# Kernel optimization log

Hardware: AMD Instinct MI355X
Metric: run time of the kernel (lower is better)

## Reference

```python
import math
import jax, jax.numpy as jnp
import numpy as np

B, N, C = 2, 2048, 768
H, DH = 12, 64  # num_heads, head_dim


def setup_inputs() -> dict:
    key = jax.random.key(0)
    ks = jax.random.split(key, 5)
    s = 1.0 / math.sqrt(C)  # keep linear outputs O(1)
    return {
        "x": jax.random.normal(ks[0], (B, N, C), jnp.float32),
        "Wq": jax.random.normal(ks[1], (C, C), jnp.float32) * s,
        "bq": jnp.zeros((C,), jnp.float32),
        "Wk": jax.random.normal(ks[2], (C, C), jnp.float32) * s,
        "bk": jnp.zeros((C,), jnp.float32),
        "Wv": jax.random.normal(ks[3], (C, C), jnp.float32) * s,
        "bv": jnp.zeros((C,), jnp.float32),
        "Wp": jax.random.normal(ks[4], (C, C), jnp.float32) * s,
        "bp": jnp.zeros((C,), jnp.float32),
    }


def reference(x, Wq, bq, Wk, bk, Wv, bv, Wp, bp):
    # Linear projections; torch nn.Linear computes x @ W.T + b, here W stored
    # as (in, out) so it's x @ W + b with equivalent math.
    def split(t):  # [B,N,C] -> [B,H,N,DH]
        return t.reshape(B, N, H, DH).transpose(0, 2, 1, 3)

    q = split(x @ Wq + bq)
    k = split(x @ Wk + bk)
    v = split(x @ Wv + bv)
    scale = 1.0 / math.sqrt(DH)
    attn = jnp.einsum("bhqd,bhkd->bhqk", q, k) * scale  # [B,H,N,N]
    attn = jax.nn.softmax(attn, axis=-1)  # attn_drop=0.0 -> identity
    y = jnp.einsum("bhqk,bhkd->bhqd", attn, v)  # [B,H,N,DH]
    y = y.transpose(0, 2, 1, 3).reshape(B, N, C)
    return y @ Wp + bp  # proj_drop=0.0 -> identity
```

## Files before the change

### kernel.cpp

```cpp
#include <hip/hip_runtime.h>


typedef __bf16 bf16_t;
typedef __bf16 bf16x8 __attribute__((ext_vector_type(8)));
typedef __bf16 bf16x4 __attribute__((ext_vector_type(4)));
typedef short  short4_t __attribute__((ext_vector_type(4)));
typedef float  floatx4 __attribute__((ext_vector_type(4)));

#define MFMA32(a, b, c) __builtin_amdgcn_mfma_f32_16x16x32_bf16(a, b, c, 0, 0, 0)
#define MFMA16(a, b, c) __builtin_amdgcn_mfma_f32_16x16x16bf16_1k(a, b, c, 0, 0, 0)

__global__ __launch_bounds__(256) void cvt_x_kernel(const float* __restrict__ x,
                                                    bf16_t* __restrict__ xb) {
  int i = blockIdx.x * 256 + threadIdx.x;
  floatx4 v = ((const floatx4*)x)[i];
  bf16x4 o;
  o[0] = (bf16_t)v[0]; o[1] = (bf16_t)v[1]; o[2] = (bf16_t)v[2]; o[3] = (bf16_t)v[3];
  ((bf16x4*)xb)[i] = o;
}

__global__ __launch_bounds__(256) void cvt_wt_kernel(
    const float* __restrict__ W0, const float* __restrict__ W1,
    const float* __restrict__ W2, const float* __restrict__ W3,
    bf16_t* __restrict__ T0, bf16_t* __restrict__ T1,
    bf16_t* __restrict__ T2, bf16_t* __restrict__ T3) {
  const int z = blockIdx.z;
  const float* W = (z == 0) ? W0 : (z == 1) ? W1 : (z == 2) ? W2 : W3;
  bf16_t* WT = (z == 0) ? T0 : (z == 1) ? T1 : (z == 2) ? T2 : T3;
  __shared__ bf16_t T[64][65];
  const int c = threadIdx.x & 63, r0 = threadIdx.x >> 6;
  const int i0 = blockIdx.y * 64, o0 = blockIdx.x * 64;
#pragma unroll
  for (int p = 0; p < 16; ++p) {
    int r = p * 4 + r0;
    T[r][c] = (bf16_t)W[(i0 + r) * 768 + o0 + c];
  }
  __syncthreads();
#pragma unroll
  for (int p = 0; p < 16; ++p) {
    int r = p * 4 + r0;
    WT[(o0 + r) * 768 + i0 + c] = T[c][r];
  }
}

#define LDPG 72


__global__ __launch_bounds__(256) void gemm_qkv(
    const bf16_t* __restrict__ Xb, const bf16_t* __restrict__ WqT,
    const bf16_t* __restrict__ WkT, const bf16_t* __restrict__ WvT,
    const float* __restrict__ bq, const float* __restrict__ bk,
    const float* __restrict__ bv, bf16_t* __restrict__ qw,
    bf16_t* __restrict__ kw, bf16_t* __restrict__ vtw) {
  __shared__ bf16_t Al[128 * LDPG];
  __shared__ bf16_t Bl[128 * LDPG];
  const int z = blockIdx.z;
  const bf16_t* Wt = (z == 0) ? WqT : (z == 1) ? WkT : WvT;
  const float* bias = (z == 0) ? bq : (z == 1) ? bk : bv;
  const float oscale = (z == 0) ? 0.18033688011112042f : 1.0f;

  const int tid = threadIdx.x, lane = tid & 63, w = tid >> 6;
  const int wr = w >> 1, wc = w & 1;
  const int l15 = lane & 15, quad = lane >> 4;
  const int m0 = blockIdx.y * 128, n0 = blockIdx.x * 128;

  floatx4 acc[4][4] = {};

  for (int kt = 0; kt < 768; kt += 64) {
#pragma unroll
    for (int p = 0; p < 4; ++p) {
      int c = p * 256 + tid;
      int row = c >> 3, qo = (c & 7) * 8;
      *(bf16x8*)&Al[row * LDPG + qo] = *(const bf16x8*)&Wt[(m0 + row) * 768 + kt + qo];
      *(bf16x8*)&Bl[row * LDPG + qo] = *(const bf16x8*)&Xb[(n0 + row) * 768 + kt + qo];
    }
    __syncthreads();
#pragma unroll
    for (int kk = 0; kk < 2; ++kk) {
      bf16x8 af[4], bfr[4];
#pragma unroll
      for (int i = 0; i < 4; ++i) {
        af[i]  = *(bf16x8*)&Al[(wr * 64 + i * 16 + l15) * LDPG + kk * 32 + quad * 8];
        bfr[i] = *(bf16x8*)&Bl[(wc * 64 + i * 16 + l15) * LDPG + kk * 32 + quad * 8];
      }
#pragma unroll
      for (int mi = 0; mi < 4; ++mi)
#pragma unroll
        for (int ni = 0; ni < 4; ++ni)
          acc[mi][ni] = MFMA32(af[mi], bfr[ni], acc[mi][ni]);
    }
    __syncthreads();
  }

  const int hh = (m0 + wr * 64) >> 6;
#pragma unroll
  for (int mi = 0; mi < 4; ++mi) {
    const int d0 = mi * 16 + quad * 4;
    const int gm0 = m0 + wr * 64 + d0;
    float bv4[4];
#pragma unroll
    for (int r = 0; r < 4; ++r) bv4[r] = bias[gm0 + r];
#pragma unroll
    for (int ni = 0; ni < 4; ++ni) {
      const int gn = n0 + wc * 64 + ni * 16 + l15;
      const int bb = gn >> 11, tok = gn & 2047;
      const int bh = bb * 12 + hh;
      if (z == 0) {
        bf16x4 pk;
#pragma unroll
        for (int r = 0; r < 4; ++r)
          pk[r] = (bf16_t)((acc[mi][ni][r] + bv4[r]) * oscale);
        *(bf16x4*)&qw[bh * 131072 + tok * 64 + d0] = pk;
      } else if (z == 1) {
        const int kt2 = tok >> 7, k128 = tok & 127;
        const int nk = k128 >> 4, kl15 = k128 & 15;
        const int kk = d0 >> 5, kq = (d0 >> 3) & 3, j0 = d0 & 7;
        bf16x4 pk;
#pragma unroll
        for (int r = 0; r < 4; ++r)
          pk[r] = (bf16_t)(acc[mi][ni][r] + bv4[r]);
        *(bf16x4*)&kw[bh * 131072 + kt2 * 8192 +
                      ((nk * 2 + kk) * 64 + kq * 16 + kl15) * 8 + j0] = pk;
      } else {
        const int kt2 = tok >> 7, k128 = tok & 127;
        const int nk = k128 >> 4, vq = (k128 >> 2) & 3, j = k128 & 3;
        const int nd = d0 >> 4, vl0 = d0 & 15;
        const int base = bh * 131072 + kt2 * 8192 +
                         ((nk * 4 + nd) * 64 + vq * 16 + vl0) * 4 + j;
#pragma unroll
        for (int r = 0; r < 4; ++r)
          vtw[base + r * 4] = (bf16_t)(acc[mi][ni][r] + bv4[r]);
      }
    }
  }
}

__global__ __launch_bounds__(256) void gemm_proj(
    const bf16_t* __restrict__ Yb, const bf16_t* __restrict__ WpT,
    const float* __restrict__ bias, float* __restrict__ out) {
  __shared__ bf16_t Al[128 * LDPG];
  __shared__ bf16_t Bl[128 * LDPG];
  const int tid = threadIdx.x, lane = tid & 63, w = tid >> 6;
  const int wr = w >> 1, wc = w & 1;
  const int l15 = lane & 15, quad = lane >> 4;
  const int m0 = blockIdx.y * 128, n0 = blockIdx.x * 128;

  floatx4 acc[4][4] = {};

  for (int kt = 0; kt < 768; kt += 64) {
#pragma unroll
    for (int p = 0; p < 4; ++p) {
      int c = p * 256 + tid;
      int row = c >> 3, qo = (c & 7) * 8;
      *(bf16x8*)&Al[row * LDPG + qo] = *(const bf16x8*)&WpT[(m0 + row) * 768 + kt + qo];
      *(bf16x8*)&Bl[row * LDPG + qo] = *(const bf16x8*)&Yb[(n0 + row) * 768 + kt + qo];
    }
    __syncthreads();
#pragma unroll
    for (int kk = 0; kk < 2; ++kk) {
      bf16x8 af[4], bfr[4];
#pragma unroll
      for (int i = 0; i < 4; ++i) {
        af[i]  = *(bf16x8*)&Al[(wr * 64 + i * 16 + l15) * LDPG + kk * 32 + quad * 8];
        bfr[i] = *(bf16x8*)&Bl[(wc * 64 + i * 16 + l15) * LDPG + kk * 32 + quad * 8];
      }
#pragma unroll
      for (int mi = 0; mi < 4; ++mi)
#pragma unroll
        for (int ni = 0; ni < 4; ++ni)
          acc[mi][ni] = MFMA32(af[mi], bfr[ni], acc[mi][ni]);
    }
    __syncthreads();
  }

#pragma unroll
  for (int mi = 0; mi < 4; ++mi) {
    const int gm0 = m0 + wr * 64 + mi * 16 + quad * 4;
    floatx4 bv4;
#pragma unroll
    for (int r = 0; r < 4; ++r) bv4[r] = bias[gm0 + r];
#pragma unroll
    for (int ni = 0; ni < 4; ++ni) {
      const int gn = n0 + wc * 64 + ni * 16 + l15;
      floatx4 v = acc[mi][ni] + bv4;
      *(floatx4*)&out[gn * 768 + gm0] = v;
    }
  }
}

__global__ __launch_bounds__(256, 4) void attn_kernel(
    const bf16_t* __restrict__ Q, const bf16_t* __restrict__ Kf,
    const bf16_t* __restrict__ Vf, bf16_t* __restrict__ Y) {
  __shared__ __align__(16) bf16_t smem[16384];
  __shared__ float Ls[2][2][2][16];
  bf16_t* Kl = smem;
  bf16_t* Vl = smem + 8192;
  float* Ox = (float*)smem;

  const int tid = threadIdx.x, lane = tid & 63, w = tid >> 6;
  const int wq = w & 1, wk = w >> 1;
  const int l15 = lane & 15, quad = lane >> 4;

  const int i = blockIdx.x;
  const int xcd = i & 7, j = i >> 3;
  const int bh = xcd * 3 + (j >> 5);
  const int q0 = (j & 31) * 64;

  const bf16_t* Qb = Q + bh * 131072;
  const bf16_t* Kb = Kf + bh * 131072;
  const bf16_t* Vb = Vf + bh * 131072;

  bf16x8 qf[2][2];
#pragma unroll
  for (int ni = 0; ni < 2; ++ni)
#pragma unroll
    for (int kk = 0; kk < 2; ++kk)
      qf[ni][kk] = *(const bf16x8*)&Qb[(q0 + wq * 32 + ni * 16 + l15) * 64 +
                                       kk * 32 + quad * 8];

  floatx4 oacc[2][4] = {};
  float lsum[2] = {0.f, 0.f};

  for (int kt = 0; kt < 16; ++kt) {
    const bf16_t* kg = Kb + kt * 8192;
    const bf16_t* vg = Vb + kt * 8192;
#pragma unroll
    for (int p = 0; p < 4; ++p) {
      const int off = (p * 256 + tid) * 8;
      *(bf16x8*)&Kl[off] = *(const bf16x8*)&kg[off];
      *(bf16x8*)&Vl[off] = *(const bf16x8*)&vg[off];
    }
    __syncthreads();

    short4_t pk[4][2];
#pragma unroll
    for (int mt = 0; mt < 4; ++mt) {
      floatx4 s[2] = {};
#pragma unroll
      for (int kk = 0; kk < 2; ++kk) {
        bf16x8 kfr = *(bf16x8*)&Kl[((wk * 4 + mt) * 2 + kk) * 512 + lane * 8];
#pragma unroll
        for (int ni = 0; ni < 2; ++ni)
          s[ni] = MFMA32(kfr, qf[ni][kk], s[ni]);
      }
#pragma unroll
      for (int ni = 0; ni < 2; ++ni) {
        bf16x4 ph;
#pragma unroll
        for (int r = 0; r < 4; ++r) {
          const float pv = __builtin_amdgcn_exp2f(s[ni][r]);
          lsum[ni] += pv;
          ph[r] = (bf16_t)pv;
        }
        pk[mt][ni] = __builtin_bit_cast(short4_t, ph);
      }
    }

#pragma unroll
    for (int mt = 0; mt < 4; ++mt)
#pragma unroll
      for (int nd = 0; nd < 4; ++nd) {
        bf16x4 vfr = *(bf16x4*)&Vl[((wk * 4 + mt) * 4 + nd) * 256 + lane * 4];
        short4_t vs = __builtin_bit_cast(short4_t, vfr);
#pragma unroll
        for (int ni = 0; ni < 2; ++ni)
          oacc[ni][nd] = MFMA16(pk[mt][ni], vs, oacc[ni][nd]);
      }
    __syncthreads();
  }

#pragma unroll
  for (int ni = 0; ni < 2; ++ni) {
    lsum[ni] += __shfl_xor(lsum[ni], 16);
    lsum[ni] += __shfl_xor(lsum[ni], 32);
  }
  if (quad == 0) {
#pragma unroll
    for (int ni = 0; ni < 2; ++ni) Ls[wq][wk][ni][l15] = lsum[ni];
  }

#pragma unroll
  for (int ni = 0; ni < 2; ++ni)
#pragma unroll
    for (int ndl = 0; ndl < 2; ++ndl) {
      const int nd = (1 - wk) * 2 + ndl;
      *(floatx4*)&Ox[((((wq * 2 + wk) * 2 + ni) * 2 + ndl) * 64 + lane) * 4] =
          oacc[ni][nd];
    }
  __syncthreads();

  const int bb = bh / 12, h = bh % 12;
#pragma unroll
  for (int ni = 0; ni < 2; ++ni) {
    float tot[4];
#pragma unroll
    for (int r = 0; r < 4; ++r)
      tot[r] = Ls[wq][0][ni][quad * 4 + r] + Ls[wq][1][ni][quad * 4 + r];
#pragma unroll
    for (int ndl = 0; ndl < 2; ++ndl) {
      const int nd = wk * 2 + ndl;
      floatx4 o = oacc[ni][nd];
      floatx4 other =
          *(floatx4*)&Ox[((((wq * 2 + (1 - wk)) * 2 + ni) * 2 + ndl) * 64 + lane) * 4];
      o += other;
#pragma unroll
      for (int r = 0; r < 4; ++r) {
        const int tok = q0 + wq * 32 + ni * 16 + quad * 4 + r;
        const int col = h * 64 + nd * 16 + l15;
        Y[(bb * 2048 + tok) * 768 + col] = (bf16_t)(o[r] / tot[r]);
      }
    }
  }
}

extern "C" void kernel_launch(void* const* d_in, const int* in_sizes, int n_in,
                              void* d_out, int out_size, void* d_ws, size_t ws_size,
                              hipStream_t stream) {
  const float* x  = (const float*)d_in[0];
  const float* Wq = (const float*)d_in[1];
  const float* bq = (const float*)d_in[2];
  const float* Wk = (const float*)d_in[3];
  const float* bk = (const float*)d_in[4];
  const float* Wv = (const float*)d_in[5];
  const float* bv = (const float*)d_in[6];
  const float* Wp = (const float*)d_in[7];
  const float* bp = (const float*)d_in[8];
  float* out = (float*)d_out;

  char* ws = (char*)d_ws;
  bf16_t* xb  = (bf16_t*)ws; ws += (size_t)4096 * 768 * 2;
  bf16_t* WqT = (bf16_t*)ws; ws += (size_t)768 * 768 * 2;
  bf16_t* WkT = (bf16_t*)ws; ws += (size_t)768 * 768 * 2;
  bf16_t* WvT = (bf16_t*)ws; ws += (size_t)768 * 768 * 2;
  bf16_t* WpT = (bf16_t*)ws; ws += (size_t)768 * 768 * 2;
  bf16_t* qw  = (bf16_t*)ws; ws += (size_t)24 * 2048 * 64 * 2;
  bf16_t* kw  = (bf16_t*)ws; ws += (size_t)24 * 2048 * 64 * 2;
  bf16_t* vtw = (bf16_t*)ws; ws += (size_t)24 * 2048 * 64 * 2;
  bf16_t* yw  = (bf16_t*)ws; ws += (size_t)4096 * 768 * 2;

  cvt_x_kernel<<<3072, 256, 0, stream>>>(x, xb);
  cvt_wt_kernel<<<dim3(12, 12, 4), 256, 0, stream>>>(Wq, Wk, Wv, Wp, WqT, WkT, WvT, WpT);

  gemm_qkv<<<dim3(32, 6, 3), 256, 0, stream>>>(xb, WqT, WkT, WvT, bq, bk, bv, qw, kw, vtw);
  attn_kernel<<<768, 256, 0, stream>>>(qw, kw, vtw, yw);
  gemm_proj<<<dim3(32, 6), 256, 0, stream>>>(yw, WpT, bp, out);
}
```

Before: 188.4 us.

## Prefetch next K/V tile into registers and compute row sums via MFMA

The attention loop now loads the next K/V tile from global memory into registers while the current tile is processed out of shared memory, so global latency overlaps with the MFMA work. The softmax row-sum is no longer a scalar accumulation of exp values; it is computed with an extra MFMA against a vector of bf16 ones, which moves that work off the VALU. Launch bounds drop from 4 to 3 waves per SIMD to make room for the extra prefetch registers. The cost is lower occupancy, and the row sum is now taken over the bf16-rounded probabilities.

```diff
diff --git a/kernel.cpp b/kernel.cpp
--- a/kernel.cpp
+++ b/kernel.cpp
@@ -188,7 +188,7 @@
   }
 }
 
-__global__ __launch_bounds__(256, 4) void attn_kernel(
+__global__ __launch_bounds__(256, 3) void attn_kernel(
     const bf16_t* __restrict__ Q, const bf16_t* __restrict__ Kf,
     const bf16_t* __restrict__ Vf, bf16_t* __restrict__ Y) {
   __shared__ __align__(16) bf16_t smem[16384];
@@ -219,19 +219,42 @@
                                        kk * 32 + quad * 8];
 
   floatx4 oacc[2][4] = {};
-  float lsum[2] = {0.f, 0.f};
-
-  for (int kt = 0; kt < 16; ++kt) {
-    const bf16_t* kg = Kb + kt * 8192;
-    const bf16_t* vg = Vb + kt * 8192;
-#pragma unroll
-    for (int p = 0; p < 4; ++p) {
-      const int off = (p * 256 + tid) * 8;
-      *(bf16x8*)&Kl[off] = *(const bf16x8*)&kg[off];
-      *(bf16x8*)&Vl[off] = *(const bf16x8*)&vg[off];
-    }
-    __syncthreads();
-
+  floatx4 sacc[2] = {};
+  const short4_t ones = {0x3F80, 0x3F80, 0x3F80, 0x3F80};
+
+  const int off0 = tid * 8, off1 = (256 + tid) * 8,
+            off2 = (512 + tid) * 8, off3 = (768 + tid) * 8;
+
+  bf16x8 ka0, ka1, ka2, ka3, va0, va1, va2, va3;
+  bf16x8 kb0, kb1, kb2, kb3, vb0, vb1, vb2, vb3;
+
+#define LOADT(K0, K1, K2, K3, V0, V1, V2, V3, KT)                \
+  {                                                              \
+    const bf16_t* kg_ = Kb + (KT) * 8192;                        \
+    const bf16_t* vg_ = Vb + (KT) * 8192;                        \
+    K0 = *(const bf16x8*)&kg_[off0];                             \
+    K1 = *(const bf16x8*)&kg_[off1];                             \
+    K2 = *(const bf16x8*)&kg_[off2];                             \
+    K3 = *(const bf16x8*)&kg_[off3];                             \
+    V0 = *(const bf16x8*)&vg_[off0];                             \
+    V1 = *(const bf16x8*)&vg_[off1];                             \
+    V2 = *(const bf16x8*)&vg_[off2];                             \
+    V3 = *(const bf16x8*)&vg_[off3];                             \
+  }
+
+#define WRITET(K0, K1, K2, K3, V0, V1, V2, V3)                   \
+  {                                                              \
+    *(bf16x8*)&Kl[off0] = K0;                                    \
+    *(bf16x8*)&Kl[off1] = K1;                                    \
+    *(bf16x8*)&Kl[off2] = K2;                                    \
+    *(bf16x8*)&Kl[off3] = K3;                                    \
+    *(bf16x8*)&Vl[off0] = V0;                                    \
+    *(bf16x8*)&Vl[off1] = V1;                                    \
+    *(bf16x8*)&Vl[off2] = V2;                                    \
+    *(bf16x8*)&Vl[off3] = V3;                                    \
+  }
+
+  auto compute = [&]() {
     short4_t pk[4][2];
 #pragma unroll
     for (int mt = 0; mt < 4; ++mt) {
@@ -247,17 +270,14 @@
       for (int ni = 0; ni < 2; ++ni) {
         bf16x4 ph;
 #pragma unroll
-        for (int r = 0; r < 4; ++r) {
-          const float pv = __builtin_amdgcn_exp2f(s[ni][r]);
-          lsum[ni] += pv;
-          ph[r] = (bf16_t)pv;
-        }
+        for (int r = 0; r < 4; ++r)
+          ph[r] = (bf16_t)__builtin_amdgcn_exp2f(s[ni][r]);
         pk[mt][ni] = __builtin_bit_cast(short4_t, ph);
       }
     }
 
 #pragma unroll
-    for (int mt = 0; mt < 4; ++mt)
+    for (int mt = 0; mt < 4; ++mt) {
 #pragma unroll
       for (int nd = 0; nd < 4; ++nd) {
         bf16x4 vfr = *(bf16x4*)&Vl[((wk * 4 + mt) * 4 + nd) * 256 + lane * 4];
@@ -266,17 +286,35 @@
         for (int ni = 0; ni < 2; ++ni)
           oacc[ni][nd] = MFMA16(pk[mt][ni], vs, oacc[ni][nd]);
       }
-    __syncthreads();
-  }
-
-#pragma unroll
-  for (int ni = 0; ni < 2; ++ni) {
-    lsum[ni] += __shfl_xor(lsum[ni], 16);
-    lsum[ni] += __shfl_xor(lsum[ni], 32);
-  }
-  if (quad == 0) {
-#pragma unroll
-    for (int ni = 0; ni < 2; ++ni) Ls[wq][wk][ni][l15] = lsum[ni];
+#pragma unroll
+      for (int ni = 0; ni < 2; ++ni)
+        sacc[ni] = MFMA16(pk[mt][ni], ones, sacc[ni]);
+    }
+  };
+
+  LOADT(ka0, ka1, ka2, ka3, va0, va1, va2, va3, 0);
+#pragma unroll
+  for (int kt = 0; kt < 16; kt += 2) {
+    WRITET(ka0, ka1, ka2, ka3, va0, va1, va2, va3);
+    __syncthreads();
+    LOADT(kb0, kb1, kb2, kb3, vb0, vb1, vb2, vb3, kt + 1);
+    compute();
+    __syncthreads();
+    WRITET(kb0, kb1, kb2, kb3, vb0, vb1, vb2, vb3);
+    __syncthreads();
+    if (kt + 2 < 16) LOADT(ka0, ka1, ka2, ka3, va0, va1, va2, va3, kt + 2);
+    compute();
+    __syncthreads();
+  }
+#undef LOADT
+#undef WRITET
+
+  if (l15 == 0) {
+#pragma unroll
+    for (int ni = 0; ni < 2; ++ni)
+#pragma unroll
+      for (int r = 0; r < 4; ++r)
+        Ls[wq][wk][ni][quad * 4 + r] = sacc[ni][r];
   }
 
 #pragma unroll
```

Result: slower. 199.9 us (+6.1%).

## Double-buffer K/V tiles via direct global-to-LDS loads and MFMA row sums

Applied to the files above, without the earlier changes.

The attention loop now works on 32-key tiles held in two LDS buffers. It loads them with global_load_lds, which writes straight into shared memory without a register round trip, so the next tile's load overlaps the current tile's compute. The softmax row sums are no longer accumulated with scalar adds and cross-lane shuffles; they are computed by an extra MFMA against a vector of bf16 ones. This adds MFMA work and a barrier on every smaller tile, and it relies on the LDS layout matching the per-thread load ordering.

```diff
diff --git a/kernel.cpp b/kernel.cpp
--- a/kernel.cpp
+++ b/kernel.cpp
@@ -9,6 +9,12 @@
 
 #define MFMA32(a, b, c) __builtin_amdgcn_mfma_f32_16x16x32_bf16(a, b, c, 0, 0, 0)
 #define MFMA16(a, b, c) __builtin_amdgcn_mfma_f32_16x16x16bf16_1k(a, b, c, 0, 0, 0)
+
+__device__ __forceinline__ void gload16(const bf16_t* g, bf16_t* l) {
+  __builtin_amdgcn_global_load_lds(
+      (__attribute__((address_space(1))) void*)g,
+      (__attribute__((address_space(3))) void*)l, 16, 0, 0);
+}
 
 __global__ __launch_bounds__(256) void cvt_x_kernel(const float* __restrict__ x,
                                                     bf16_t* __restrict__ xb) {
@@ -193,8 +199,6 @@
     const bf16_t* __restrict__ Vf, bf16_t* __restrict__ Y) {
   __shared__ __align__(16) bf16_t smem[16384];
   __shared__ float Ls[2][2][2][16];
-  bf16_t* Kl = smem;
-  bf16_t* Vl = smem + 8192;
   float* Ox = (float*)smem;
 
   const int tid = threadIdx.x, lane = tid & 63, w = tid >> 6;
@@ -207,8 +211,8 @@
   const int q0 = (j & 31) * 64;
 
   const bf16_t* Qb = Q + bh * 131072;
-  const bf16_t* Kb = Kf + bh * 131072;
-  const bf16_t* Vb = Vf + bh * 131072;
+  const bf16_t* Kg = Kf + bh * 131072 + tid * 8;
+  const bf16_t* Vg = Vf + bh * 131072 + tid * 8;
 
   bf16x8 qf[2][2];
 #pragma unroll
@@ -219,26 +223,30 @@
                                        kk * 32 + quad * 8];
 
   floatx4 oacc[2][4] = {};
-  float lsum[2] = {0.f, 0.f};
-
-  for (int kt = 0; kt < 16; ++kt) {
-    const bf16_t* kg = Kb + kt * 8192;
-    const bf16_t* vg = Vb + kt * 8192;
-#pragma unroll
-    for (int p = 0; p < 4; ++p) {
-      const int off = (p * 256 + tid) * 8;
-      *(bf16x8*)&Kl[off] = *(const bf16x8*)&kg[off];
-      *(bf16x8*)&Vl[off] = *(const bf16x8*)&vg[off];
-    }
-    __syncthreads();
-
-    short4_t pk[4][2];
-#pragma unroll
-    for (int mt = 0; mt < 4; ++mt) {
+  floatx4 sacc[2] = {};
+  const short4_t ones = {0x3F80, 0x3F80, 0x3F80, 0x3F80};
+
+  auto stage = [&](int b, int t) {
+    const bf16_t* kg = Kg + t * 4096;
+    const bf16_t* vg = Vg + t * 4096;
+    bf16_t* kl = smem + b * 8192 + tid * 8;
+    bf16_t* vl = smem + b * 8192 + 4096 + tid * 8;
+    gload16(kg, kl);
+    gload16(kg + 2048, kl + 2048);
+    gload16(vg, vl);
+    gload16(vg + 2048, vl + 2048);
+  };
+
+  auto compute = [&](int b) {
+    const bf16_t* Kl = smem + b * 8192;
+    const bf16_t* Vl = smem + b * 8192 + 4096;
+    short4_t pk[2][2];
+#pragma unroll
+    for (int mt = 0; mt < 2; ++mt) {
       floatx4 s[2] = {};
 #pragma unroll
       for (int kk = 0; kk < 2; ++kk) {
-        bf16x8 kfr = *(bf16x8*)&Kl[((wk * 4 + mt) * 2 + kk) * 512 + lane * 8];
+        bf16x8 kfr = *(const bf16x8*)&Kl[((wk * 2 + mt) * 2 + kk) * 512 + lane * 8];
 #pragma unroll
         for (int ni = 0; ni < 2; ++ni)
           s[ni] = MFMA32(kfr, qf[ni][kk], s[ni]);
@@ -247,36 +255,44 @@
       for (int ni = 0; ni < 2; ++ni) {
         bf16x4 ph;
 #pragma unroll
-        for (int r = 0; r < 4; ++r) {
-          const float pv = __builtin_amdgcn_exp2f(s[ni][r]);
-          lsum[ni] += pv;
-          ph[r] = (bf16_t)pv;
-        }
+        for (int r = 0; r < 4; ++r)
+          ph[r] = (bf16_t)__builtin_amdgcn_exp2f(s[ni][r]);
         pk[mt][ni] = __builtin_bit_cast(short4_t, ph);
       }
     }
-
-#pragma unroll
-    for (int mt = 0; mt < 4; ++mt)
+#pragma unroll
+    for (int mt = 0; mt < 2; ++mt) {
 #pragma unroll
       for (int nd = 0; nd < 4; ++nd) {
-        bf16x4 vfr = *(bf16x4*)&Vl[((wk * 4 + mt) * 4 + nd) * 256 + lane * 4];
+        bf16x4 vfr = *(const bf16x4*)&Vl[((wk * 2 + mt) * 4 + nd) * 256 + lane * 4];
         short4_t vs = __builtin_bit_cast(short4_t, vfr);
 #pragma unroll
         for (int ni = 0; ni < 2; ++ni)
           oacc[ni][nd] = MFMA16(pk[mt][ni], vs, oacc[ni][nd]);
       }
-    __syncthreads();
-  }
-
-#pragma unroll
-  for (int ni = 0; ni < 2; ++ni) {
-    lsum[ni] += __shfl_xor(lsum[ni], 16);
-    lsum[ni] += __shfl_xor(lsum[ni], 32);
-  }
-  if (quad == 0) {
-#pragma unroll
-    for (int ni = 0; ni < 2; ++ni) Ls[wq][wk][ni][l15] = lsum[ni];
+#pragma unroll
+      for (int ni = 0; ni < 2; ++ni)
+        sacc[ni] = MFMA16(pk[mt][ni], ones, sacc[ni]);
+    }
+  };
+
+  stage(0, 0);
+  __syncthreads();
+  for (int t = 0; t < 32; t += 2) {
+    stage(1, t + 1);
+    compute(0);
+    __syncthreads();
+    if (t + 2 < 32) stage(0, t + 2);
+    compute(1);
+    __syncthreads();
+  }
+
+  if (l15 == 0) {
+#pragma unroll
+    for (int ni = 0; ni < 2; ++ni)
+#pragma unroll
+      for (int r = 0; r < 4; ++r)
+        Ls[wq][wk][ni][quad * 4 + r] = sacc[ni][r];
   }
 
 #pragma unroll
```

Result: no change. 187.2 us (-0.6%).
